# Optimization experiments

Measured on AMD Instinct MI355X. Metric: run time of the kernel, lower is better.

Reference implementation:

```python
import jax, jax.numpy as jnp
import numpy as np

N_BINS = 10


def setup_inputs() -> dict:
    key = jax.random.key(0)
    k1, k2 = jax.random.split(key)
    N, C = 131072, 1000
    logits = jax.random.normal(k1, (N, C), dtype=jnp.float32)
    labels = jax.random.randint(k2, (N,), 0, C, dtype=jnp.int64)
    return {"logits": logits, "labels": labels}


def reference(logits, labels):
    N, C = logits.shape
    probs = jax.nn.softmax(logits, axis=1)  # [N, C]
    # bin b covers (b/n_bins, (b+1)/n_bins]: value v -> ceil(v*n_bins)-1, clipped
    bins = jnp.clip(jnp.ceil(probs * N_BINS).astype(jnp.int32) - 1, 0, N_BINS - 1)
    valid = probs > 0.0  # torch uses gt(lower): exactly-0 confidences fall in no bin
    # flatten (class, bin) -> single segment id
    seg = (bins + jnp.arange(C, dtype=jnp.int32)[None, :] * N_BINS).reshape(-1)
    w = valid.reshape(-1).astype(probs.dtype)
    cnt = jax.ops.segment_sum(w, seg, num_segments=C * N_BINS)
    sum_conf = jax.ops.segment_sum((probs * valid).reshape(-1), seg, num_segments=C * N_BINS)
    correct = (labels[:, None] == jnp.arange(C, dtype=labels.dtype)[None, :]) & valid
    sum_acc = jax.ops.segment_sum(correct.reshape(-1).astype(probs.dtype), seg, num_segments=C * N_BINS)
    prop_in_bin = cnt / N
    safe_cnt = jnp.where(cnt > 0, cnt, 1.0)
    gap = jnp.abs(sum_conf / safe_cnt - sum_acc / safe_cnt)
    per_bin = jnp.where(cnt > 0, gap * prop_in_bin, 0.0)  # [C*n_bins]
    per_class_sce = per_bin.reshape(C, N_BINS).sum(axis=1)  # [C]
    return jnp.mean(per_class_sce).reshape(-1)
```

## Files before the change

### kernel.cpp

```cpp
#include <hip/hip_runtime.h>
#include <math.h>

#define CLS 1000
#define NB 10
#define HIST (CLS * NB)
#define TPB 256
#define WPB (TPB / 64)
#define GRID 768
#define NWAVE (GRID * WPB)

#define WAITVM(n) asm volatile("s_waitcnt vmcnt(" #n ")" ::: "memory")

__global__ void ece_init_kernel(float* conf_g, unsigned* acc_g) {
    int i = blockIdx.x * blockDim.x + threadIdx.x;
    if (i < HIST) {
        conf_g[i] = 0.0f;
        acc_g[i]  = 0u;
    }
}

__device__ __forceinline__ void stage_row(const float* __restrict__ logits,
                                          int row, float* dst, int lane)
{
    const float* src = logits + (size_t)row * CLS + 4 * lane;
    #pragma unroll
    for (int k = 0; k < 3; ++k) {
        __builtin_amdgcn_global_load_lds(
            (const __attribute__((address_space(1))) unsigned int*)(src + 256 * k),
            (__attribute__((address_space(3))) unsigned int*)(dst + 256 * k),
            16, 0, 0);
    }
    __builtin_amdgcn_global_load_lds(
        (const __attribute__((address_space(1))) unsigned int*)(src + 744),
        (__attribute__((address_space(3))) unsigned int*)(dst + 768),
        16, 0, 0);
}

__global__ __launch_bounds__(TPB, 4) void ece_hist_kernel(
    const float* __restrict__ logits, const int* __restrict__ labels,
    float* __restrict__ conf_g, unsigned* __restrict__ acc_g, int N)
{
    __shared__ float stage_s[WPB * 3 * 1024];

    const int lane = threadIdx.x & 63;
    const int wib  = threadIdx.x >> 6;
    const int gw   = blockIdx.x * WPB + wib;
    const int nw   = NWAVE;

    float* slice = &stage_s[wib * 3072];

    float racc[16];
    #pragma unroll
    for (int j = 0; j < 16; ++j) racc[j] = 0.0f;

    if (gw < N)      stage_row(logits, gw,      slice,        lane);
    if (gw + nw < N) stage_row(logits, gw + nw, slice + 1024, lane);

    int cur = 0;
    for (int r = gw; r < N; r += nw) {
        const int rn2 = r + 2 * nw;
        if (rn2 < N) {
            int b2 = cur + 2; if (b2 >= 3) b2 -= 3;
            stage_row(logits, rn2, slice + b2 * 1024, lane);
            WAITVM(8);
        } else if (r + nw < N) {
            WAITVM(4);
        } else {
            WAITVM(0);
        }
        __builtin_amdgcn_sched_barrier(0);

        float* bufp = slice + cur * 1024;
        const int lab = labels[r];

        float p[16];
        #pragma unroll
        for (int k = 0; k < 4; ++k) {
            int idx = (k < 3) ? (k * 256 + 4 * lane)
                              : (792 + 4 * ((lane < 58) ? lane : 0));
            float4 v = *(const float4*)&bufp[idx];
            p[4 * k + 0] = v.x; p[4 * k + 1] = v.y;
            p[4 * k + 2] = v.z; p[4 * k + 3] = v.w;
        }

        #pragma unroll
        for (int j = 0; j < 16; ++j) {
            float e = __expf(p[j]);
            if (j >= 12) {
                int c = 768 + 4 * lane + (j & 3);
                e = (c < CLS) ? e : 0.0f;
            }
            p[j] = e;
        }
        float t0 = (p[0] + p[1]) + (p[2] + p[3]);
        float t1 = (p[4] + p[5]) + (p[6] + p[7]);
        float t2 = (p[8] + p[9]) + (p[10] + p[11]);
        float t3 = (p[12] + p[13]) + (p[14] + p[15]);
        float s  = (t0 + t1) + (t2 + t3);
        #pragma unroll
        for (int off = 32; off; off >>= 1) s += __shfl_xor(s, off);
        const float inv = 1.0f / s;

        float qmax = 0.0f;
        #pragma unroll
        for (int j = 0; j < 16; ++j) {
            float q = p[j] * inv;
            p[j] = q;
            qmax = fmaxf(qmax, q);
            racc[j] += (q <= 0.1f) ? q : 0.0f;
        }
        if (__any(qmax > 0.1f)) {
            #pragma unroll
            for (int j = 0; j < 16; ++j) {
                float q = p[j];
                if (q > 0.1f) {
                    int c  = 256 * (j >> 2) + 4 * lane + (j & 3);
                    int bb = (int)ceilf(q * (float)NB) - 1;
                    bb = bb < 0 ? 0 : (bb > NB - 1 ? NB - 1 : bb);
                    atomicAdd(&conf_g[bb * CLS + c], q);
                }
            }
        }

        const int li = (lab >= 768) ? lab + 24 : lab;
        float xl = bufp[li];
        float ql = __expf(xl) * inv;
        if (lane == 0 && ql > 0.0f) {
            int bb = 0;
            if (ql > 0.1f) {
                bb = (int)ceilf(ql * (float)NB) - 1;
                bb = bb > NB - 1 ? NB - 1 : bb;
            }
            atomicAdd(&acc_g[bb * CLS + lab], 1u);
        }

        cur = (cur + 1 == 3) ? 0 : cur + 1;
    }

    __syncthreads();
    for (int i = threadIdx.x; i < CLS; i += blockDim.x) stage_s[i] = 0.0f;
    __syncthreads();
    #pragma unroll
    for (int j = 0; j < 16; ++j) {
        int c = 256 * (j >> 2) + 4 * lane + (j & 3);
        if (c < CLS && racc[j] != 0.0f) atomicAdd(&stage_s[c], racc[j]);
    }
    __syncthreads();
    for (int i = threadIdx.x; i < CLS; i += blockDim.x) {
        float v = stage_s[i];
        if (v != 0.0f) atomicAdd(&conf_g[i], v);
    }
}

__global__ void ece_final_kernel(const float* __restrict__ conf_g,
                                 const unsigned* __restrict__ acc_g,
                                 float* __restrict__ out, int N)
{
    __shared__ double wsum[16];
    double s = 0.0;
    for (int i = threadIdx.x; i < HIST; i += blockDim.x) {
        s += fabs((double)conf_g[i] - (double)acc_g[i]);
    }
    #pragma unroll
    for (int off = 32; off; off >>= 1) s += __shfl_xor(s, off);
    int lane = threadIdx.x & 63, w = threadIdx.x >> 6;
    if (lane == 0) wsum[w] = s;
    __syncthreads();
    if (threadIdx.x == 0) {
        double t = 0.0;
        int nwv = blockDim.x >> 6;
        for (int i = 0; i < nwv; ++i) t += wsum[i];
        out[0] = (float)(t / ((double)N * (double)CLS));
    }
}

extern "C" void kernel_launch(void* const* d_in, const int* in_sizes, int n_in,
                              void* d_out, int out_size, void* d_ws, size_t ws_size,
                              hipStream_t stream) {
    const float* logits = (const float*)d_in[0];
    const int*   labels = (const int*)d_in[1];
    const int N = in_sizes[1];

    float*    conf_g = (float*)d_ws;
    unsigned* acc_g  = (unsigned*)((char*)d_ws + HIST * sizeof(float));
    float*    out    = (float*)d_out;

    ece_init_kernel<<<(HIST + 255) / 256, 256, 0, stream>>>(conf_g, acc_g);
    ece_hist_kernel<<<GRID, TPB, 0, stream>>>(logits, labels, conf_g, acc_g, N);
    ece_final_kernel<<<1, 1024, 0, stream>>>(conf_g, acc_g, out, N);
}
```

Baseline: 129.2 us.

## Mix LDS-staged and register-prefetched rows in a three-row software pipeline

Replaces the triple LDS staging buffer with two LDS buffers plus one row prefetched directly into registers, processing three rows per unrolled loop iteration. This cuts LDS use per wave, and the grid grows from 768 to 1024 blocks to raise occupancy and the number of loads in flight. The cost is more register pressure and a more intricate vmcnt accounting. The waitcnt values must stay correct with the mix of LDS-direct loads and register loads, and the tail handling now covers up to four leftover rows.

After: 138.4 us. 7.1% more time.

```diff
diff --git a/kernel.cpp b/kernel.cpp
--- a/kernel.cpp
+++ b/kernel.cpp
@@ -6,10 +6,11 @@
 #define HIST (CLS * NB)
 #define TPB 256
 #define WPB (TPB / 64)
-#define GRID 768
+#define GRID 1024
 #define NWAVE (GRID * WPB)
 
 #define WAITVM(n) asm volatile("s_waitcnt vmcnt(" #n ")" ::: "memory")
+#define SCHEDB()  __builtin_amdgcn_sched_barrier(0)
 
 __global__ void ece_init_kernel(float* conf_g, unsigned* acc_g) {
     int i = blockIdx.x * blockDim.x + threadIdx.x;
@@ -36,105 +37,165 @@
         16, 0, 0);
 }
 
+__device__ __forceinline__ void lds_row(const float* bufp, int lane, float p[16])
+{
+    #pragma unroll
+    for (int k = 0; k < 4; ++k) {
+        int idx = (k < 3) ? (k * 256 + 4 * lane)
+                          : (792 + 4 * ((lane < 58) ? lane : 0));
+        float4 v = *(const float4*)&bufp[idx];
+        p[4 * k + 0] = v.x; p[4 * k + 1] = v.y;
+        p[4 * k + 2] = v.z; p[4 * k + 3] = v.w;
+    }
+}
+
+__device__ __forceinline__ void reg_row(const float* __restrict__ logits,
+                                        int row, int lane, float p[16])
+{
+    const float* src = logits + (size_t)row * CLS;
+    #pragma unroll
+    for (int k = 0; k < 3; ++k) {
+        float4 v = *(const float4*)(src + 256 * k + 4 * lane);
+        p[4 * k + 0] = v.x; p[4 * k + 1] = v.y;
+        p[4 * k + 2] = v.z; p[4 * k + 3] = v.w;
+    }
+    int cl = (lane < 58) ? lane : 0;
+    float4 v = *(const float4*)(src + 768 + 4 * cl);
+    p[12] = v.x; p[13] = v.y; p[14] = v.z; p[15] = v.w;
+}
+
+__device__ __forceinline__ void process_row(float p[16], float xl, int lane,
+                                            int lab, float racc[16],
+                                            float* __restrict__ conf_g,
+                                            unsigned* __restrict__ acc_g)
+{
+    #pragma unroll
+    for (int j = 0; j < 16; ++j) {
+        float e = __expf(p[j]);
+        if (j >= 12) {
+            int c = 768 + 4 * lane + (j & 3);
+            e = (c < CLS) ? e : 0.0f;
+        }
+        p[j] = e;
+    }
+    float t0 = (p[0] + p[1]) + (p[2] + p[3]);
+    float t1 = (p[4] + p[5]) + (p[6] + p[7]);
+    float t2 = (p[8] + p[9]) + (p[10] + p[11]);
+    float t3 = (p[12] + p[13]) + (p[14] + p[15]);
+    float s  = (t0 + t1) + (t2 + t3);
+    #pragma unroll
+    for (int off = 32; off; off >>= 1) s += __shfl_xor(s, off);
+    const float inv = 1.0f / s;
+
+    float qmax = 0.0f;
+    #pragma unroll
+    for (int j = 0; j < 16; ++j) {
+        float q = p[j] * inv;
+        p[j] = q;
+        qmax = fmaxf(qmax, q);
+        racc[j] += (q <= 0.1f) ? q : 0.0f;
+    }
+    if (__any(qmax > 0.1f)) {
+        #pragma unroll
+        for (int j = 0; j < 16; ++j) {
+            float q = p[j];
+            if (q > 0.1f) {
+                int c  = 256 * (j >> 2) + 4 * lane + (j & 3);
+                int bb = (int)ceilf(q * (float)NB) - 1;
+                bb = bb < 0 ? 0 : (bb > NB - 1 ? NB - 1 : bb);
+                atomicAdd(&conf_g[bb * CLS + c], q);
+            }
+        }
+    }
+
+    float ql = __expf(xl) * inv;
+    if (lane == 0 && ql > 0.0f) {
+        int bb = 0;
+        if (ql > 0.1f) {
+            bb = (int)ceilf(ql * (float)NB) - 1;
+            bb = bb > NB - 1 ? NB - 1 : bb;
+        }
+        atomicAdd(&acc_g[bb * CLS + lab], 1u);
+    }
+}
+
 __global__ __launch_bounds__(TPB, 4) void ece_hist_kernel(
     const float* __restrict__ logits, const int* __restrict__ labels,
     float* __restrict__ conf_g, unsigned* __restrict__ acc_g, int N)
 {
-    __shared__ float stage_s[WPB * 3 * 1024];
+    __shared__ float stage_s[WPB * 2 * 1024];
 
     const int lane = threadIdx.x & 63;
     const int wib  = threadIdx.x >> 6;
     const int gw   = blockIdx.x * WPB + wib;
     const int nw   = NWAVE;
 
-    float* slice = &stage_s[wib * 3072];
+    float* A = &stage_s[wib * 2048];
+    float* B = A + 1024;
 
     float racc[16];
     #pragma unroll
     for (int j = 0; j < 16; ++j) racc[j] = 0.0f;
 
-    if (gw < N)      stage_row(logits, gw,      slice,        lane);
-    if (gw + nw < N) stage_row(logits, gw + nw, slice + 1024, lane);
-
-    int cur = 0;
-    for (int r = gw; r < N; r += nw) {
-        const int rn2 = r + 2 * nw;
-        if (rn2 < N) {
-            int b2 = cur + 2; if (b2 >= 3) b2 -= 3;
-            stage_row(logits, rn2, slice + b2 * 1024, lane);
-            WAITVM(8);
-        } else if (r + nw < N) {
-            WAITVM(4);
+    int r = gw;
+    if (r < N)      stage_row(logits, r,      A, lane);
+    if (r + nw < N) stage_row(logits, r + nw, B, lane);
+
+    while (r + 4 * nw < N) {
+        float c[16];
+        reg_row(logits, r + 2 * nw, lane, c);
+        SCHEDB();
+        WAITVM(8);
+        SCHEDB();
+        {
+            const int lab = labels[r];
+            float p[16];
+            lds_row(A, lane, p);
+            float xl = A[(lab >= 768) ? lab + 24 : lab];
+            process_row(p, xl, lane, lab, racc, conf_g, acc_g);
+        }
+        stage_row(logits, r + 3 * nw, A, lane);
+        SCHEDB();
+        WAITVM(8);
+        SCHEDB();
+        {
+            const int lab = labels[r + nw];
+            float p[16];
+            lds_row(B, lane, p);
+            float xl = B[(lab >= 768) ? lab + 24 : lab];
+            process_row(p, xl, lane, lab, racc, conf_g, acc_g);
+        }
+        stage_row(logits, r + 4 * nw, B, lane);
+        SCHEDB();
+        WAITVM(8);
+        SCHEDB();
+        {
+            const int r2  = r + 2 * nw;
+            const int lab = labels[r2];
+            float xl = logits[(size_t)r2 * CLS + lab];
+            process_row(c, xl, lane, lab, racc, conf_g, acc_g);
+        }
+        r += 3 * nw;
+    }
+
+    int idx = 0;
+    for (; r < N; r += nw, ++idx) {
+        const int lab = labels[r];
+        float p[16];
+        float xl;
+        if (idx == 0) {
+            WAITVM(0);
+            SCHEDB();
+            lds_row(A, lane, p);
+            xl = A[(lab >= 768) ? lab + 24 : lab];
+        } else if (idx == 1) {
+            lds_row(B, lane, p);
+            xl = B[(lab >= 768) ? lab + 24 : lab];
         } else {
-            WAITVM(0);
-        }
-        __builtin_amdgcn_sched_barrier(0);
-
-        float* bufp = slice + cur * 1024;
-        const int lab = labels[r];
-
-        float p[16];
-        #pragma unroll
-        for (int k = 0; k < 4; ++k) {
-            int idx = (k < 3) ? (k * 256 + 4 * lane)
-                              : (792 + 4 * ((lane < 58) ? lane : 0));
-            float4 v = *(const float4*)&bufp[idx];
-            p[4 * k + 0] = v.x; p[4 * k + 1] = v.y;
-            p[4 * k + 2] = v.z; p[4 * k + 3] = v.w;
-        }
-
-        #pragma unroll
-        for (int j = 0; j < 16; ++j) {
-            float e = __expf(p[j]);
-            if (j >= 12) {
-                int c = 768 + 4 * lane + (j & 3);
-                e = (c < CLS) ? e : 0.0f;
-            }
-            p[j] = e;
-        }
-        float t0 = (p[0] + p[1]) + (p[2] + p[3]);
-        float t1 = (p[4] + p[5]) + (p[6] + p[7]);
-        float t2 = (p[8] + p[9]) + (p[10] + p[11]);
-        float t3 = (p[12] + p[13]) + (p[14] + p[15]);
-        float s  = (t0 + t1) + (t2 + t3);
-        #pragma unroll
-        for (int off = 32; off; off >>= 1) s += __shfl_xor(s, off);
-        const float inv = 1.0f / s;
-
-        float qmax = 0.0f;
-        #pragma unroll
-        for (int j = 0; j < 16; ++j) {
-            float q = p[j] * inv;
-            p[j] = q;
-            qmax = fmaxf(qmax, q);
-            racc[j] += (q <= 0.1f) ? q : 0.0f;
-        }
-        if (__any(qmax > 0.1f)) {
-            #pragma unroll
-            for (int j = 0; j < 16; ++j) {
-                float q = p[j];
-                if (q > 0.1f) {
-                    int c  = 256 * (j >> 2) + 4 * lane + (j & 3);
-                    int bb = (int)ceilf(q * (float)NB) - 1;
-                    bb = bb < 0 ? 0 : (bb > NB - 1 ? NB - 1 : bb);
-                    atomicAdd(&conf_g[bb * CLS + c], q);
-                }
-            }
-        }
-
-        const int li = (lab >= 768) ? lab + 24 : lab;
-        float xl = bufp[li];
-        float ql = __expf(xl) * inv;
-        if (lane == 0 && ql > 0.0f) {
-            int bb = 0;
-            if (ql > 0.1f) {
-                bb = (int)ceilf(ql * (float)NB) - 1;
-                bb = bb > NB - 1 ? NB - 1 : bb;
-            }
-            atomicAdd(&acc_g[bb * CLS + lab], 1u);
-        }
-
-        cur = (cur + 1 == 3) ? 0 : cur + 1;
+            reg_row(logits, r, lane, p);
+            xl = logits[(size_t)r * CLS + lab];
+        }
+        process_row(p, xl, lane, lab, racc, conf_g, acc_g);
     }
 
     __syncthreads();
```

## Replace LDS triple-buffered async staging with register double-buffered loads

Applied to the files above, without the earlier changes.

Removes the global_load_lds staging ring of three rows per wave with explicit vmcnt waits. Each wave now prefetches the next row directly into registers (double buffering) and reads the label logit straight from global memory. Shared memory drops to a 1000-float accumulator, and grid size and occupancy hint are raised to rely on more waves for latency hiding. The trade is a shallower prefetch depth and higher register pressure in exchange for more resident waves.

Measured after the change: 139.5 us. 1.08x slower.

```diff
diff --git a/kernel.cpp b/kernel.cpp
--- a/kernel.cpp
+++ b/kernel.cpp
@@ -6,10 +6,8 @@
 #define HIST (CLS * NB)
 #define TPB 256
 #define WPB (TPB / 64)
-#define GRID 768
+#define GRID 1280
 #define NWAVE (GRID * WPB)
-
-#define WAITVM(n) asm volatile("s_waitcnt vmcnt(" #n ")" ::: "memory")
 
 __global__ void ece_init_kernel(float* conf_g, unsigned* acc_g) {
     int i = blockIdx.x * blockDim.x + threadIdx.x;
@@ -19,69 +17,50 @@
     }
 }
 
-__device__ __forceinline__ void stage_row(const float* __restrict__ logits,
-                                          int row, float* dst, int lane)
+__device__ __forceinline__ void load_row(const float* __restrict__ logits,
+                                         int row, int lane, float p[16])
 {
-    const float* src = logits + (size_t)row * CLS + 4 * lane;
+    const float* src = logits + (size_t)row * CLS;
     #pragma unroll
     for (int k = 0; k < 3; ++k) {
-        __builtin_amdgcn_global_load_lds(
-            (const __attribute__((address_space(1))) unsigned int*)(src + 256 * k),
-            (__attribute__((address_space(3))) unsigned int*)(dst + 256 * k),
-            16, 0, 0);
+        float4 v = *(const float4*)(src + 256 * k + 4 * lane);
+        p[4 * k + 0] = v.x; p[4 * k + 1] = v.y;
+        p[4 * k + 2] = v.z; p[4 * k + 3] = v.w;
     }
-    __builtin_amdgcn_global_load_lds(
-        (const __attribute__((address_space(1))) unsigned int*)(src + 744),
-        (__attribute__((address_space(3))) unsigned int*)(dst + 768),
-        16, 0, 0);
+    int cl = (lane < 58) ? lane : 0;
+    float4 v = *(const float4*)(src + 768 + 4 * cl);
+    p[12] = v.x; p[13] = v.y; p[14] = v.z; p[15] = v.w;
 }
 
-__global__ __launch_bounds__(TPB, 4) void ece_hist_kernel(
+__global__ __launch_bounds__(TPB, 5) void ece_hist_kernel(
     const float* __restrict__ logits, const int* __restrict__ labels,
     float* __restrict__ conf_g, unsigned* __restrict__ acc_g, int N)
 {
-    __shared__ float stage_s[WPB * 3 * 1024];
+    __shared__ float conf0_s[CLS];
+
+    for (int i = threadIdx.x; i < CLS; i += blockDim.x) conf0_s[i] = 0.0f;
+    __syncthreads();
 
     const int lane = threadIdx.x & 63;
     const int wib  = threadIdx.x >> 6;
     const int gw   = blockIdx.x * WPB + wib;
     const int nw   = NWAVE;
 
-    float* slice = &stage_s[wib * 3072];
-
     float racc[16];
     #pragma unroll
     for (int j = 0; j < 16; ++j) racc[j] = 0.0f;
 
-    if (gw < N)      stage_row(logits, gw,      slice,        lane);
-    if (gw + nw < N) stage_row(logits, gw + nw, slice + 1024, lane);
+    float p[16];
+    int r = gw;
+    if (r < N) load_row(logits, r, lane, p);
 
-    int cur = 0;
-    for (int r = gw; r < N; r += nw) {
-        const int rn2 = r + 2 * nw;
-        if (rn2 < N) {
-            int b2 = cur + 2; if (b2 >= 3) b2 -= 3;
-            stage_row(logits, rn2, slice + b2 * 1024, lane);
-            WAITVM(8);
-        } else if (r + nw < N) {
-            WAITVM(4);
-        } else {
-            WAITVM(0);
-        }
-        __builtin_amdgcn_sched_barrier(0);
+    for (; r < N; r += nw) {
+        const int rn = r + nw;
+        float b[16];
+        if (rn < N) load_row(logits, rn, lane, b);
 
-        float* bufp = slice + cur * 1024;
         const int lab = labels[r];
-
-        float p[16];
-        #pragma unroll
-        for (int k = 0; k < 4; ++k) {
-            int idx = (k < 3) ? (k * 256 + 4 * lane)
-                              : (792 + 4 * ((lane < 58) ? lane : 0));
-            float4 v = *(const float4*)&bufp[idx];
-            p[4 * k + 0] = v.x; p[4 * k + 1] = v.y;
-            p[4 * k + 2] = v.z; p[4 * k + 3] = v.w;
-        }
+        const float xl = logits[(size_t)r * CLS + lab];
 
         #pragma unroll
         for (int j = 0; j < 16; ++j) {
@@ -122,8 +101,6 @@
             }
         }
 
-        const int li = (lab >= 768) ? lab + 24 : lab;
-        float xl = bufp[li];
         float ql = __expf(xl) * inv;
         if (lane == 0 && ql > 0.0f) {
             int bb = 0;
@@ -134,20 +111,19 @@
             atomicAdd(&acc_g[bb * CLS + lab], 1u);
         }
 
-        cur = (cur + 1 == 3) ? 0 : cur + 1;
+        #pragma unroll
+        for (int j = 0; j < 16; ++j) p[j] = b[j];
     }
 
-    __syncthreads();
-    for (int i = threadIdx.x; i < CLS; i += blockDim.x) stage_s[i] = 0.0f;
     __syncthreads();
     #pragma unroll
     for (int j = 0; j < 16; ++j) {
         int c = 256 * (j >> 2) + 4 * lane + (j & 3);
-        if (c < CLS && racc[j] != 0.0f) atomicAdd(&stage_s[c], racc[j]);
+        if (c < CLS && racc[j] != 0.0f) atomicAdd(&conf0_s[c], racc[j]);
     }
     __syncthreads();
     for (int i = threadIdx.x; i < CLS; i += blockDim.x) {
-        float v = stage_s[i];
+        float v = conf0_s[i];
         if (v != 0.0f) atomicAdd(&conf_g[i], v);
     }
 }
```
